# Kernel optimization log

Measured on AMD Instinct MI355X. Metric: run time of the kernel, lower is better.

The kernel has to match this reference:

```python
import jax, jax.numpy as jnp
import numpy as np
from functools import partial

V = 40          # vocab: 38 labels + EOS + SOS
E = 512         # embedding dim
H = 512         # rnn hidden dim == key_dim
DK = 512        # key dim
DV = 512        # value dim
T_ENC = 8192    # encoder time steps
MAX_LEN = 200
EOS_IDX = 38    # index of '$' appended after the 38 base labels


def setup_inputs() -> dict:
    key = jax.random.key(0)
    ks = jax.random.split(key, 9)
    s = 0.05
    return {
        "encoding": jax.random.normal(ks[0], (1, T_ENC, DK + DV), dtype=jnp.float32),
        "hidden":   jax.random.normal(ks[1], (1, H), dtype=jnp.float32),
        "embed":    jax.random.normal(ks[2], (V, E), dtype=jnp.float32) * s,
        "w_ih":     jax.random.normal(ks[3], (3 * H, E), dtype=jnp.float32) * s,
        "w_hh":     jax.random.normal(ks[4], (3 * H, H), dtype=jnp.float32) * s,
        "b_ih":     jnp.zeros((3 * H,), dtype=jnp.float32),
        "b_hh":     jnp.zeros((3 * H,), dtype=jnp.float32),
        "w_out":    jax.random.normal(ks[5], (V, DV + H), dtype=jnp.float32) * s,
        "b_out":    jnp.zeros((V,), dtype=jnp.float32),
    }


def _gru_cell(x, h, w_ih, w_hh, b_ih, b_hh):
    # torch GRUCell math. x: [E], h: [H]
    gi = w_ih @ x + b_ih            # [3H]
    gh = w_hh @ h + b_hh            # [3H]
    i_r, i_z, i_n = jnp.split(gi, 3)
    h_r, h_z, h_n = jnp.split(gh, 3)
    r = jax.nn.sigmoid(i_r + h_r)
    z = jax.nn.sigmoid(i_z + h_z)
    n = jnp.tanh(i_n + r * h_n)
    return (1.0 - z) * n + z * h


def reference(encoding, hidden, embed, w_ih, w_hh, b_ih, b_hh, w_out, b_out):
    keys = encoding[0, :, :DK]      # [T, DK]
    values = encoding[0, :, DK:]    # [T, DV]
    scale = 1.0 / jnp.sqrt(jnp.float32(DK))

    y0 = embed[EOS_IDX]             # decode seeded with EOS embedding
    h0 = hidden[0]                  # [H]

    def step(carry, _):
        y_prev, h = carry
        h = _gru_cell(y_prev, h, w_ih, w_hh, b_ih, b_hh)        # query [H]
        scores = jax.nn.softmax((keys @ h) * scale)              # [T] dot attention
        summary = scores @ values                                # [DV]
        out = w_out @ jnp.concatenate([summary, h]) + b_out      # [V]
        probs = jax.nn.softmax(out)
        best = jnp.argmax(probs)
        return (embed[best], h), (out, scores, best)

    (_, _), (outs, attns, bests) = jax.lax.scan(step, (y0, h0), None, length=MAX_LEN)

    outputs = outs[None]            # [1, MAX_LEN, V]
    attentions = attns[None]        # [1, MAX_LEN, T]
    # emitted length = first step whose argmax is EOS (original early-exits there)
    is_eos = bests == EOS_IDX
    lens = jnp.where(jnp.any(is_eos), jnp.argmax(is_eos), MAX_LEN).astype(jnp.int64 if jax.config.jax_enable_x64 else jnp.int32)[None]
    return outputs, lens, attentions
```

## Files before the change

### kernel.cpp

```cpp
#include <hip/hip_runtime.h>
#include <math.h>


#define NV      40
#define TENC    8192
#define MAXLEN  200
#define EOS_IDX 38
#define NB      256
#define NT      1024
#define NW      16
#define ROWS    32
#define NG      64
#define GSTRIDE 192
#define CREP    64
#define HPOFF   (NG * GSTRIDE)
#define SLOT    (HPOFF + 64)
#define SCALE   0.04419417382415922f

#define WS_ACC  128
#define WS_GH   (WS_ACC + 3 * SLOT)
#define WS_GI   (WS_GH + 3 * 1536)

__device__ __forceinline__ int ld_ai(int* p) {
  return __hip_atomic_load(p, __ATOMIC_RELAXED, __HIP_MEMORY_SCOPE_AGENT);
}
__device__ __forceinline__ float ld_af(float* p) {
  return __hip_atomic_load(p, __ATOMIC_RELAXED, __HIP_MEMORY_SCOPE_AGENT);
}
__device__ __forceinline__ void st_af(float* p, float v) {
  __hip_atomic_store(p, v, __ATOMIC_RELAXED, __HIP_MEMORY_SCOPE_AGENT);
}
__device__ __forceinline__ void st_ai(int* p, int v) {
  __hip_atomic_store(p, v, __ATOMIC_RELAXED, __HIP_MEMORY_SCOPE_AGENT);
}
__device__ __forceinline__ void add_relaxed(int* p) {
  __hip_atomic_fetch_add(p, 1, __ATOMIC_RELAXED, __HIP_MEMORY_SCOPE_AGENT);
}
__device__ __forceinline__ int ld_lds_acq(int* p) {
  return __hip_atomic_load(p, __ATOMIC_ACQUIRE, __HIP_MEMORY_SCOPE_WORKGROUP);
}
__device__ __forceinline__ void st_lds_rel(int* p, int v) {
  __hip_atomic_store(p, v, __ATOMIC_RELEASE, __HIP_MEMORY_SCOPE_WORKGROUP);
}
__device__ __forceinline__ void inc_lds_rel(int* p) {
  __hip_atomic_fetch_add(p, 1, __ATOMIC_RELEASE, __HIP_MEMORY_SCOPE_WORKGROUP);
}

__device__ __forceinline__ float wred(float s) {
#pragma unroll
  for (int o = 32; o > 0; o >>= 1) s += __shfl_xor(s, o, 64);
  return s;
}
__device__ __forceinline__ float dot8(float4 a0, float4 a1, float4 b0,
                                      float4 b1) {
  return a0.x * b0.x + a0.y * b0.y + a0.z * b0.z + a0.w * b0.w +
         a1.x * b1.x + a1.y * b1.y + a1.z * b1.z + a1.w * b1.w;
}
__device__ __forceinline__ float wdot512(const float* __restrict__ a,
                                         const float* __restrict__ b) {
  const int l = threadIdx.x & 63;
  const float4 a0 = ((const float4*)a)[l];
  const float4 a1 = ((const float4*)a)[l + 64];
  const float4 b0 = ((const float4*)b)[l];
  const float4 b1 = ((const float4*)b)[l + 64];
  return wred(dot8(a0, a1, b0, b1));
}

__global__ void dec_init(int* wsi) {
  for (int k = threadIdx.x; k < WS_GH; k += NT) wsi[k] = 0;
}

__global__ void __launch_bounds__(NT, 4) dec_main(
    const float* __restrict__ enc, const float* __restrict__ hidden,
    const float* __restrict__ embed, const float* __restrict__ w_ih,
    const float* __restrict__ w_hh, const float* __restrict__ b_ih,
    const float* __restrict__ b_hh, const float* __restrict__ w_out,
    const float* __restrict__ b_out, float* __restrict__ o,
    float* __restrict__ ws) {
  const int b = blockIdx.x, tid = threadIdx.x;
  const int wave = tid >> 6, lane = tid & 63;
  const int g = b & (NG - 1);
  const int rep = b & 7;
  const int r0 = b * ROWS;

  __shared__ __align__(16) float h_lds[512];
  __shared__ float pw_lds[NW * 48];
  __shared__ float sc_lds[1];
  __shared__ int go_lds;
  __shared__ int bf_lds;
  __shared__ int pwc;

  if (tid < 512) h_lds[tid] = hidden[tid];
  if (tid == 0) { go_lds = 0; bf_lds = -1; pwc = 0; }

  for (int u = wave; u < 240; u += NW) {
    const int gl = b * 240 + u;
    const int v = gl / 1536, j = gl - v * 1536;
    const float d = wdot512(w_ih + (size_t)j * 512, embed + (size_t)v * 512);
    if (lane == 0) ws[WS_GI + (size_t)v * 1536 + j] = d + b_ih[j];
  }
  for (int jr = wave; jr < 6; jr += NW) {
    const int j = b * 6 + jr;
    const float d = wdot512(w_hh + (size_t)j * 512, hidden);
    if (lane == 0) st_af(&ws[WS_GH + 2 * 1536 + j], d + b_hh[j]);
  }
  __syncthreads();
  if (tid == 0) {
    int* cbase = (int*)(ws + WS_ACC + 2 * SLOT + g * GSTRIDE + CREP);
#pragma unroll
    for (int r = 0; r < 8; ++r) add_relaxed(cbase + 16 * r);
  }

  const float* k0p = enc + (size_t)(r0 + 2 * wave) * 1024;
  const float4 k0a = ((const float4*)k0p)[lane];
  const float4 k0b = ((const float4*)k0p)[lane + 64];
  const float4 k1a = ((const float4*)(k0p + 1024))[lane];
  const float4 k1b = ((const float4*)(k0p + 1024))[lane + 64];

  float Mr0 = (lane == 40) ? 1.0f : 0.0f, Mr1 = Mr0;
  {
    const float* v0p = k0p + 512;
    const float4 va0 = ((const float4*)v0p)[lane];
    const float4 va1 = ((const float4*)v0p)[lane + 64];
    const float4 vb0 = ((const float4*)(v0p + 1024))[lane];
    const float4 vb1 = ((const float4*)(v0p + 1024))[lane + 64];
    for (int v = 0; v < NV; ++v) {
      const float* wp = w_out + (size_t)v * 1024;
      const float4 w0 = ((const float4*)wp)[lane];
      const float4 w1 = ((const float4*)wp)[lane + 64];
      const float sa = wred(dot8(va0, va1, w0, w1));
      const float sb = wred(dot8(vb0, vb1, w0, w1));
      if (lane == v) { Mr0 = sa; Mr1 = sb; }
    }
  }
  float4 xa0 = {0, 0, 0, 0}, xa1 = {0, 0, 0, 0};
  float xb = 0.0f;
  if (wave >= 1 && wave <= 6) {
    const int j = b * 6 + (wave - 1);
    const float* wp = w_hh + (size_t)j * 512;
    xa0 = ((const float4*)wp)[lane];
    xa1 = ((const float4*)wp)[lane + 64];
    xb = b_hh[j];
  } else if (wave == 7 && b >= 1 && b <= NV) {
    const float* wp = w_out + (size_t)(b - 1) * 1024 + 512;
    xa0 = ((const float4*)wp)[lane];
    xa1 = ((const float4*)wp)[lane + 64];
    xb = b_out[b - 1];
  }

  int eos_reg = -1;
  float p0 = 0.0f, p1 = 0.0f;
  float* attn = o + (size_t)MAXLEN * NV + 1;

  for (int t = 0; t <= MAXLEN; ++t) {
    if (wave == 0) {
      float* accs = ws + WS_ACC + ((t + 2) % 3) * SLOT;
      {
        int* cp = (int*)(accs + lane * GSTRIDE + CREP + 16 * rep);
        bool ok = false;
        for (;;) {
          if (!ok) ok = (ld_ai(cp) >= NB / NG);
          if (__ballot(!ok) == 0ull) break;
          __builtin_amdgcn_s_sleep(1);
        }
      }
      if (lane == 0) st_lds_rel(&go_lds, t + 1);
      if (t > 0) {
        const float hp = (lane < NV) ? ld_af(&accs[HPOFF + lane]) : 0.0f;
        float c0 = 0, c1 = 0, c2 = 0, c3 = 0;
#pragma unroll
        for (int q = 0; q < NG / 4; ++q) {
          c0 += ld_af(&accs[(4 * q + 0) * GSTRIDE + lane]);
          c1 += ld_af(&accs[(4 * q + 1) * GSTRIDE + lane]);
          c2 += ld_af(&accs[(4 * q + 2) * GSTRIDE + lane]);
          c3 += ld_af(&accs[(4 * q + 3) * GSTRIDE + lane]);
        }
        const float cs = (c0 + c1) + (c2 + c3);
        const float S = __shfl(cs, NV, 64);
        const float ov = cs * (1.0f / S) + hp;
        unsigned long long key = 0ull;
        if (lane < NV) {
          unsigned u = __float_as_uint(ov);
          u = (u & 0x80000000u) ? ~u : (u | 0x80000000u);
          key = ((unsigned long long)u << 32) | (unsigned)(~lane);
        }
#pragma unroll
        for (int m = 32; m > 0; m >>= 1) {
          const unsigned long long k2 = __shfl_xor(key, m, 64);
          if (k2 > key) key = k2;
        }
        const int best = (int)(~(unsigned)key);
        if (b == 0 && lane < NV) o[(size_t)(t - 1) * NV + lane] = ov;
        if (lane == 0) {
          sc_lds[0] = S;
          if (b == 0) {
            if (best == EOS_IDX && eos_reg < 0) eos_reg = t - 1;
            if (t == MAXLEN)
              o[(size_t)MAXLEN * NV] =
                  (eos_reg < 0) ? (float)MAXLEN : (float)eos_reg;
          }
          st_lds_rel(&bf_lds, (t << 6) | best);
        }
      } else if (lane == 0) {
        st_lds_rel(&bf_lds, EOS_IDX);
      }
    } else if (wave >= 8 && t < MAXLEN) {
      const int j = tid - 512;
      while (ld_lds_acq(&go_lds) < t + 1) __builtin_amdgcn_s_sleep(1);
      float* ghs = ws + WS_GH + ((t + 2) % 3) * 1536;
      const float ghr = ld_af(&ghs[j]);
      const float ghz = ld_af(&ghs[j + 512]);
      const float ghn = ld_af(&ghs[j + 1024]);
      int bf;
      while (((bf = ld_lds_acq(&bf_lds)) >> 6) < t) __builtin_amdgcn_s_sleep(1);
      const float* gi = ws + WS_GI + (size_t)(bf & 63) * 1536;
      const float gir = gi[j], giz = gi[j + 512], gin = gi[j + 1024];
      const float r = 1.0f / (1.0f + expf(-(gir + ghr)));
      const float z = 1.0f / (1.0f + expf(-(giz + ghz)));
      const float n = tanhf(gin + r * ghn);
      h_lds[j] = (1.0f - z) * n + z * h_lds[j];
    }
    __syncthreads();

    if (t > 0 && lane < 2)
      attn[(size_t)(t - 1) * TENC + r0 + 2 * wave + lane] =
          (lane ? p1 : p0) * (1.0f / sc_lds[0]);
    if (t == MAXLEN) break;

    {
      const float4 hh0 = ((const float4*)h_lds)[lane];
      const float4 hh1 = ((const float4*)h_lds)[lane + 64];
      const float d0 = wred(dot8(k0a, k0b, hh0, hh1));
      const float d1 = wred(dot8(k1a, k1b, hh0, hh1));
      p0 = expf(d0 * SCALE);
      p1 = expf(d1 * SCALE);
      const float fold = p0 * Mr0 + p1 * Mr1;
      if (wave == 0) {
        while (ld_lds_acq(&pwc) < 15 * (t + 1)) __builtin_amdgcn_s_sleep(1);
        float s = fold;
#pragma unroll
        for (int w2 = 1; w2 < NW; ++w2) s += pw_lds[w2 * 48 + lane];
        if (lane < 41)
          atomicAdd(&ws[WS_ACC + (t % 3) * SLOT + g * GSTRIDE + lane], s);
      } else {
        if (lane < 41) pw_lds[wave * 48 + lane] = fold;
        if (lane == 0) inc_lds_rel(&pwc);
        if (wave >= 1 && wave <= 6) {
          const float d = wred(dot8(xa0, xa1, hh0, hh1));
          if (lane == 0)
            st_af(&ws[WS_GH + (t % 3) * 1536 + b * 6 + (wave - 1)], d + xb);
        } else if (wave == 7 && b >= 1 && b <= NV) {
          const float d = wred(dot8(xa0, xa1, hh0, hh1));
          if (lane == 0)
            st_af(&ws[WS_ACC + (t % 3) * SLOT + HPOFF + (b - 1)], d + xb);
        } else if (wave == 15 && b < NG) {
          float* nx = ws + WS_ACC + ((t + 1) % 3) * SLOT + b * GSTRIDE;
          if (lane < 41) st_af(&nx[lane], 0.0f);
          else if (lane >= 48 && lane < 56)
            st_ai((int*)&nx[CREP + 16 * (lane - 48)], 0);
        }
      }
    }
    __syncthreads();

    if (tid == 0) {
      int* cbase = (int*)(ws + WS_ACC + (t % 3) * SLOT + g * GSTRIDE + CREP);
#pragma unroll
      for (int r = 0; r < 8; ++r) add_relaxed(cbase + 16 * r);
    }
  }
}

extern "C" void kernel_launch(void* const* d_in, const int* in_sizes, int n_in,
                              void* d_out, int out_size, void* d_ws,
                              size_t ws_size, hipStream_t stream) {
  const float* enc    = (const float*)d_in[0];
  const float* hidden = (const float*)d_in[1];
  const float* embed  = (const float*)d_in[2];
  const float* w_ih   = (const float*)d_in[3];
  const float* w_hh   = (const float*)d_in[4];
  const float* b_ih   = (const float*)d_in[5];
  const float* b_hh   = (const float*)d_in[6];
  const float* w_out  = (const float*)d_in[7];
  const float* b_out  = (const float*)d_in[8];
  float* out = (float*)d_out;
  float* ws  = (float*)d_ws;

  dec_init<<<dim3(1), dim3(NT), 0, stream>>>((int*)d_ws);
  dec_main<<<dim3(NB), dim3(NT), 0, stream>>>(enc, hidden, embed, w_ih, w_hh,
                                              b_ih, b_hh, w_out, b_out, out,
                                              ws);
}
```

Baseline: 988.6 us.

## Replicate cross-block accumulators four ways to spread global read contention

Each group's partial-sum accumulators and the hidden-projection values are now written into four replicated copies. Each block then reads back from the copy chosen by its low block-index bits, so the 256 blocks polling the same addresses are spread across four regions. The aim is to cut L2 and atomic hotspot contention on the per-step reduction read. In exchange, every step issues four times as many atomic adds and stores, and zeroing the next slot costs more.

```diff
diff --git a/kernel.cpp b/kernel.cpp
--- a/kernel.cpp
+++ b/kernel.cpp
@@ -11,10 +11,10 @@
 #define NW      16
 #define ROWS    32
 #define NG      64
-#define GSTRIDE 192
-#define CREP    64
+#define GSTRIDE 320
+#define CREP    192
 #define HPOFF   (NG * GSTRIDE)
-#define SLOT    (HPOFF + 64)
+#define SLOT    (HPOFF + 256)
 #define SCALE   0.04419417382415922f
 
 #define WS_ACC  128
@@ -81,6 +81,8 @@
   const int wave = tid >> 6, lane = tid & 63;
   const int g = b & (NG - 1);
   const int rep = b & 7;
+  const int dsel = (b & 3) * 48;
+  const int hsel = (b & 3) * 64;
   const int r0 = b * ROWS;
 
   __shared__ __align__(16) float h_lds[512];
@@ -166,14 +168,14 @@
       }
       if (lane == 0) st_lds_rel(&go_lds, t + 1);
       if (t > 0) {
-        const float hp = (lane < NV) ? ld_af(&accs[HPOFF + lane]) : 0.0f;
+        const float hp = (lane < NV) ? ld_af(&accs[HPOFF + hsel + lane]) : 0.0f;
         float c0 = 0, c1 = 0, c2 = 0, c3 = 0;
 #pragma unroll
         for (int q = 0; q < NG / 4; ++q) {
-          c0 += ld_af(&accs[(4 * q + 0) * GSTRIDE + lane]);
-          c1 += ld_af(&accs[(4 * q + 1) * GSTRIDE + lane]);
-          c2 += ld_af(&accs[(4 * q + 2) * GSTRIDE + lane]);
-          c3 += ld_af(&accs[(4 * q + 3) * GSTRIDE + lane]);
+          c0 += ld_af(&accs[(4 * q + 0) * GSTRIDE + dsel + lane]);
+          c1 += ld_af(&accs[(4 * q + 1) * GSTRIDE + dsel + lane]);
+          c2 += ld_af(&accs[(4 * q + 2) * GSTRIDE + dsel + lane]);
+          c3 += ld_af(&accs[(4 * q + 3) * GSTRIDE + dsel + lane]);
         }
         const float cs = (c0 + c1) + (c2 + c3);
         const float S = __shfl(cs, NV, 64);
@@ -240,8 +242,13 @@
         float s = fold;
 #pragma unroll
         for (int w2 = 1; w2 < NW; ++w2) s += pw_lds[w2 * 48 + lane];
-        if (lane < 41)
-          atomicAdd(&ws[WS_ACC + (t % 3) * SLOT + g * GSTRIDE + lane], s);
+        if (lane < 41) {
+          float* base = ws + WS_ACC + (t % 3) * SLOT + g * GSTRIDE + lane;
+          atomicAdd(base, s);
+          atomicAdd(base + 48, s);
+          atomicAdd(base + 96, s);
+          atomicAdd(base + 144, s);
+        }
       } else {
         if (lane < 41) pw_lds[wave * 48 + lane] = fold;
         if (lane == 0) inc_lds_rel(&pwc);
@@ -251,13 +258,23 @@
             st_af(&ws[WS_GH + (t % 3) * 1536 + b * 6 + (wave - 1)], d + xb);
         } else if (wave == 7 && b >= 1 && b <= NV) {
           const float d = wred(dot8(xa0, xa1, hh0, hh1));
-          if (lane == 0)
-            st_af(&ws[WS_ACC + (t % 3) * SLOT + HPOFF + (b - 1)], d + xb);
+          if (lane == 0) {
+            float* hb = ws + WS_ACC + (t % 3) * SLOT + HPOFF + (b - 1);
+            st_af(hb, d + xb);
+            st_af(hb + 64, d + xb);
+            st_af(hb + 128, d + xb);
+            st_af(hb + 192, d + xb);
+          }
         } else if (wave == 15 && b < NG) {
           float* nx = ws + WS_ACC + ((t + 1) % 3) * SLOT + b * GSTRIDE;
-          if (lane < 41) st_af(&nx[lane], 0.0f);
-          else if (lane >= 48 && lane < 56)
+          if (lane < 41) {
+            st_af(&nx[lane], 0.0f);
+            st_af(&nx[48 + lane], 0.0f);
+            st_af(&nx[96 + lane], 0.0f);
+            st_af(&nx[144 + lane], 0.0f);
+          } else if (lane >= 48 && lane < 56) {
             st_ai((int*)&nx[CREP + 16 * (lane - 48)], 0);
+          }
         }
       }
     }
```

Result: slower. 3.538 ms (+257.9%).
